# Optimization experiments

Hardware: AMD Instinct MI355X
Metric: run time of the kernel (lower is better)

Reference implementation:

```python
import jax, jax.numpy as jnp
import numpy as np

B, H, L = 8, 512, 8192


def setup_inputs() -> dict:
    key = jax.random.key(0)
    k1, k2, k3, k4 = jax.random.split(key, 4)
    u = jax.random.normal(k1, (B, H, L), dtype=jnp.float32)
    # SSM convolution kernel (decaying, as a Vandermonde 'Vr' kernel would be)
    decay = jnp.exp(-jnp.arange(L, dtype=jnp.float32) / 512.0)  # (L,)
    K = jax.random.normal(k2, (H, L), dtype=jnp.float32) * decay[None, :] / np.sqrt(L)
    D = jax.random.normal(k3, (H,), dtype=jnp.float32)
    W_mix = jax.random.normal(k4, (H, H), dtype=jnp.float32) / np.sqrt(H)
    return {"u": u, "K": K, "D": D, "W_mix": W_mix}


def reference(u, K, D, W_mix):
    # FFTConvReservoir: causal conv of u (B,H,L) with per-channel kernel K (H,L)
    n = 2 * L  # zero-pad to avoid circular wrap-around
    Uf = jnp.fft.rfft(u, n=n, axis=-1)            # (B,H,L+1) complex
    Kf = jnp.fft.rfft(K, n=n, axis=-1)            # (H,L+1) complex
    y = jnp.fft.irfft(Uf * Kf[None], n=n, axis=-1)[..., :L]
    y = y + D[None, :, None] * u                  # skip connection
    # LinearReservoir mix (frozen real matrix) applied pointwise over time
    y = jnp.einsum('ph,bhl->bpl', W_mix, y)
    # tanh nonlinearity
    y = jnp.tanh(y)
    return y
```

## Files before the change

### kernel.cpp

```cpp
#include <hip/hip_runtime.h>
#include <hip/hip_fp16.h>


#define FFT_N 8192
#define TAPS  4096
#define Bb 8
#define Hh 512
#define Ll 8192
#define NTHR 512

#define P(i) ((i) ^ (((i) >> 4) & 15))

__host__ __device__ constexpr int clog2(int x) { return x <= 1 ? 0 : 1 + clog2(x >> 1); }

typedef _Float16 half8 __attribute__((ext_vector_type(8)));
typedef _Float16 half2v __attribute__((ext_vector_type(2)));
typedef float f32x4 __attribute__((ext_vector_type(4)));

__device__ __forceinline__ float2 cmul(float2 a, float2 b) {
    return make_float2(a.x * b.x - a.y * b.y, a.x * b.y + a.y * b.x);
}
__device__ __forceinline__ float2 cmulc(float2 a, float2 b) {
    return make_float2(a.x * b.x + a.y * b.y, a.y * b.x - a.x * b.y);
}
__device__ __forceinline__ float2 cadd(float2 a, float2 b) { return make_float2(a.x + b.x, a.y + b.y); }
__device__ __forceinline__ float2 csub(float2 a, float2 b) { return make_float2(a.x - b.x, a.y - b.y); }

__device__ __forceinline__ float tanh_fast(float x) {
    float e = __expf(2.0f * x);
    return 1.0f - 2.0f / (e + 1.0f);
}

__device__ __forceinline__ void r4_fwd(float2& x0, float2& x1, float2& x2, float2& x3,
                                       float2 w1, float2 w2, float2 w3) {
    float2 t0 = cadd(x0, x2), t1 = csub(x0, x2), t2 = cadd(x1, x3), t3 = csub(x1, x3);
    x0 = cadd(t0, t2);
    x1 = cmul(make_float2(t1.x + t3.y, t1.y - t3.x), w1);
    x2 = cmul(csub(t0, t2), w2);
    x3 = cmul(make_float2(t1.x - t3.y, t1.y + t3.x), w3);
}
__device__ __forceinline__ void r4_fwd_nt(float2& x0, float2& x1, float2& x2, float2& x3) {
    float2 t0 = cadd(x0, x2), t1 = csub(x0, x2), t2 = cadd(x1, x3), t3 = csub(x1, x3);
    x0 = cadd(t0, t2);
    x1 = make_float2(t1.x + t3.y, t1.y - t3.x);
    x2 = csub(t0, t2);
    x3 = make_float2(t1.x - t3.y, t1.y + t3.x);
}
__device__ __forceinline__ void r4_inv(float2& x0, float2& x1, float2& x2, float2& x3,
                                       float2 w1, float2 w2, float2 w3) {
    float2 u1 = cmulc(x1, w1), u2 = cmulc(x2, w2), u3 = cmulc(x3, w3);
    float2 s0 = cadd(x0, u2), s2 = csub(x0, u2), s1 = cadd(u1, u3);
    float2 d = csub(u1, u3);
    float2 s3 = make_float2(-d.y, d.x);
    x0 = cadd(s0, s1); x1 = cadd(s2, s3); x2 = csub(s0, s1); x3 = csub(s2, s3);
}
__device__ __forceinline__ void r4_inv_nt(float2& x0, float2& x1, float2& x2, float2& x3) {
    float2 s0 = cadd(x0, x2), s2 = csub(x0, x2), s1 = cadd(x1, x3);
    float2 d = csub(x1, x3);
    float2 s3 = make_float2(-d.y, d.x);
    x0 = cadd(s0, s1); x1 = cadd(s2, s3); x2 = csub(s0, s1); x3 = csub(s2, s3);
}

template<int Q, int NT>
__device__ __forceinline__ void fwd_super(float2* buf, const float2* __restrict__ tw, int tid) {
    constexpr int q2 = Q / 4;
    constexpr int NB = 2048 / Q;
    constexpr int L2Q2 = clog2(q2);
    #pragma unroll 1
    for (int g = tid; g < 512; g += NT) {
        const int j = g & (q2 - 1);
        const int Bi = g >> L2Q2;
        const int base = Bi * 4 * Q + j;
        float2 x[4][4];
        #pragma unroll
        for (int a = 0; a < 4; ++a)
            #pragma unroll
            for (int b = 0; b < 4; ++b)
                x[a][b] = buf[P(base + a * Q + b * q2)];
        #pragma unroll
        for (int b = 0; b < 4; ++b) {
            float2 w1 = tw[(j + b * q2) * NB];
            float2 w2 = cmul(w1, w1), w3 = cmul(w2, w1);
            r4_fwd(x[0][b], x[1][b], x[2][b], x[3][b], w1, w2, w3);
        }
        {
            float2 v1 = tw[j * 4 * NB];
            float2 v2 = cmul(v1, v1), v3 = cmul(v2, v1);
            #pragma unroll
            for (int a = 0; a < 4; ++a)
                r4_fwd(x[a][0], x[a][1], x[a][2], x[a][3], v1, v2, v3);
        }
        #pragma unroll
        for (int a = 0; a < 4; ++a)
            #pragma unroll
            for (int b = 0; b < 4; ++b)
                buf[P(base + a * Q + b * q2)] = x[a][b];
    }
}

template<int Q, int NT>
__device__ __forceinline__ void inv_super(float2* buf, const float2* __restrict__ tw, int tid) {
    constexpr int q2 = Q / 4;
    constexpr int NB = 2048 / Q;
    constexpr int L2Q2 = clog2(q2);
    #pragma unroll 1
    for (int g = tid; g < 512; g += NT) {
        const int j = g & (q2 - 1);
        const int Bi = g >> L2Q2;
        const int base = Bi * 4 * Q + j;
        float2 x[4][4];
        #pragma unroll
        for (int a = 0; a < 4; ++a)
            #pragma unroll
            for (int b = 0; b < 4; ++b)
                x[a][b] = buf[P(base + a * Q + b * q2)];
        {
            float2 v1 = tw[j * 4 * NB];
            float2 v2 = cmul(v1, v1), v3 = cmul(v2, v1);
            #pragma unroll
            for (int a = 0; a < 4; ++a)
                r4_inv(x[a][0], x[a][1], x[a][2], x[a][3], v1, v2, v3);
        }
        #pragma unroll
        for (int b = 0; b < 4; ++b) {
            float2 w1 = tw[(j + b * q2) * NB];
            float2 w2 = cmul(w1, w1), w3 = cmul(w2, w1);
            r4_inv(x[0][b], x[1][b], x[2][b], x[3][b], w1, w2, w3);
        }
        #pragma unroll
        for (int a = 0; a < 4; ++a)
            #pragma unroll
            for (int b = 0; b < 4; ++b)
                buf[P(base + a * Q + b * q2)] = x[a][b];
    }
}

template<int NT>
__device__ __forceinline__ void mid_stage(float2* buf, const float2* __restrict__ kf, int tid) {
    const float2 W1[4] = {{1.f, 0.f}, {0.92387953f, -0.38268343f}, {0.70710678f, -0.70710678f}, {0.38268343f, -0.92387953f}};
    const float2 W2[4] = {{1.f, 0.f}, {0.70710678f, -0.70710678f}, {0.f, -1.f}, {-0.70710678f, -0.70710678f}};
    const float2 W3[4] = {{1.f, 0.f}, {0.38268343f, -0.92387953f}, {-0.70710678f, -0.70710678f}, {-0.92387953f, 0.38268343f}};
    #pragma unroll 1
    for (int g = tid; g < 512; g += NT) {
        const int base = 16 * g;
        float2 x[16];
        #pragma unroll
        for (int i = 0; i < 16; ++i) x[i] = buf[P(base + i)];
        #pragma unroll
        for (int b = 0; b < 4; ++b)
            r4_fwd(x[b], x[4 + b], x[8 + b], x[12 + b], W1[b], W2[b], W3[b]);
        #pragma unroll
        for (int a = 0; a < 4; ++a)
            r4_fwd_nt(x[4 * a], x[4 * a + 1], x[4 * a + 2], x[4 * a + 3]);
        const float4* kp = reinterpret_cast<const float4*>(kf + base);
        #pragma unroll
        for (int i = 0; i < 8; ++i) {
            float4 kv = kp[i];
            x[2 * i]     = cmul(x[2 * i],     make_float2(kv.x, kv.y));
            x[2 * i + 1] = cmul(x[2 * i + 1], make_float2(kv.z, kv.w));
        }
        #pragma unroll
        for (int a = 0; a < 4; ++a)
            r4_inv_nt(x[4 * a], x[4 * a + 1], x[4 * a + 2], x[4 * a + 3]);
        #pragma unroll
        for (int b = 0; b < 4; ++b)
            r4_inv(x[b], x[4 + b], x[8 + b], x[12 + b], W1[b], W2[b], W3[b]);
        #pragma unroll
        for (int i = 0; i < 16; ++i) buf[P(base + i)] = x[i];
    }
}

__global__ __launch_bounds__(256) void tw_init_kernel(float2* __restrict__ tw) {
    int k = blockIdx.x * 256 + threadIdx.x;
    if (k < FFT_N) {
        float s, c;
        sincospif(-(float)k / 4096.0f, &s, &c);
        tw[k] = make_float2(c, s);
    }
}

__global__ __launch_bounds__(256) void wh_kernel(const float* __restrict__ W, _Float16* __restrict__ Wh) {
    int i = blockIdx.x * 256 + threadIdx.x;
    Wh[i] = (_Float16)W[i];
}

__global__ __launch_bounds__(NTHR) void kf_kernel(const float* __restrict__ K,
                                                  const float* __restrict__ D,
                                                  const float2* __restrict__ tw,
                                                  float2* __restrict__ Kf) {
    __shared__ float2 buf[FFT_N];
    const int h = blockIdx.x;
    const int tid = threadIdx.x;
    for (int k = 0; k < 8; ++k) {
        int t = tid + k * NTHR;
        float va = (t < TAPS) ? K[(size_t)h * Ll + t] : 0.0f;
        if (t == 0) va += D[h];
        float2 a = make_float2(va, 0.0f);
        buf[P(t)] = a;
        buf[P(t + 4096)] = cmul(a, tw[t]);
    }
    __syncthreads();
    fwd_super<1024, NTHR>(buf, tw, tid);
    __syncthreads();
    fwd_super<64, NTHR>(buf, tw, tid);
    __syncthreads();
    fwd_super<4, NTHR>(buf, tw, tid);
    __syncthreads();
    for (int k = 0; k < 16; ++k) {
        int idx = tid + k * NTHR;
        Kf[(size_t)h * FFT_N + idx] = buf[P(idx)];
    }
}

__global__ __launch_bounds__(NTHR) void conv_kernel(const float* __restrict__ u,
                                                    const float2* __restrict__ Kf,
                                                    const float2* __restrict__ tw,
                                                    _Float16* __restrict__ yh) {
    __shared__ float2 buf[FFT_N];
    const int bid = blockIdx.x;
    const int h = bid & 511;
    const int pc = bid >> 9;
    const int c = pc & 1;
    const int bp = pc >> 1;
    const int b0 = bp * 2, b1 = b0 + 1;
    const int tid = threadIdx.x;
    const float* u0 = u + ((size_t)b0 * Hh + h) * Ll;
    const float* u1 = u + ((size_t)b1 * Hh + h) * Ll;
    const int t0 = c * 4096 - 4096;

    for (int k = 0; k < 8; ++k) {
        int t = tid + k * NTHR;
        int ta = t0 + t;
        float2 a = make_float2(0.f, 0.f);
        if (ta >= 0) a = make_float2(u0[ta], u1[ta]);
        int tb = ta + 4096;
        float2 bv = make_float2(u0[tb], u1[tb]);
        buf[P(t)] = cadd(a, bv);
        buf[P(t + 4096)] = cmul(csub(a, bv), tw[t]);
    }
    __syncthreads();
    fwd_super<1024, NTHR>(buf, tw, tid);
    __syncthreads();
    fwd_super<64, NTHR>(buf, tw, tid);
    __syncthreads();
    mid_stage<NTHR>(buf, Kf + (size_t)h * FFT_N, tid);
    __syncthreads();
    inv_super<64, NTHR>(buf, tw, tid);
    __syncthreads();
    inv_super<1024, NTHR>(buf, tw, tid);
    __syncthreads();

    const float scale = 1.0f / (float)FFT_N;
    _Float16* y0 = yh + ((size_t)b0 * Hh + h) * Ll;
    _Float16* y1 = yh + ((size_t)b1 * Hh + h) * Ll;
    for (int k = 0; k < 4; ++k) {
        int t = 2 * (tid + k * NTHR);
        float2 a0 = buf[P(t)],     c0 = buf[P(t + 4096)];
        float2 a1 = buf[P(t + 1)], c1 = buf[P(t + 4097)];
        float2 o0 = csub(a0, cmulc(c0, tw[t]));
        float2 o1 = csub(a1, cmulc(c1, tw[t + 1]));
        int l = c * 4096 + t;
        half2v h0, h1;
        h0.x = (_Float16)(o0.x * scale); h0.y = (_Float16)(o1.x * scale);
        h1.x = (_Float16)(o0.y * scale); h1.y = (_Float16)(o1.y * scale);
        *(half2v*)(y0 + l) = h0;
        *(half2v*)(y1 + l) = h1;
    }
}

__global__ __launch_bounds__(256) void transpose_kernel(const unsigned short* __restrict__ yh,
                                                        unsigned short* __restrict__ yt) {
    const int tid = threadIdx.x;
    const int b = blockIdx.z;
    const int h_base = blockIdx.y * 64 + (tid & 7) * 8;
    const int l_base = blockIdx.x * 256 + (tid >> 3) * 8;

    uint4 in[8];
    #pragma unroll
    for (int r = 0; r < 8; ++r)
        in[r] = *(const uint4*)(yh + (size_t)(b * Hh + h_base + r) * Ll + l_base);

    #pragma unroll
    for (int cp = 0; cp < 8; ++cp) {
        uint4 o;
        unsigned* ow = (unsigned*)&o;
        #pragma unroll
        for (int w = 0; w < 4; ++w) {
            unsigned lo = ((const unsigned*)&in[2 * w])[cp >> 1];
            unsigned hi = ((const unsigned*)&in[2 * w + 1])[cp >> 1];
            if (cp & 1) ow[w] = (lo >> 16) | (hi & 0xffff0000u);
            else        ow[w] = (lo & 0xffffu) | (hi << 16);
        }
        *(uint4*)(yt + ((size_t)b * Ll + l_base + cp) * Hh + h_base) = o;
    }
}

__global__ __launch_bounds__(256, 4) void mix_kernel(const _Float16* __restrict__ Wh,
                                                     const _Float16* __restrict__ yt,
                                                     float* __restrict__ out) {
    __shared__ _Float16 As[256 * 64];
    __shared__ _Float16 Bs[64 * 64];
    const int tid = threadIdx.x;
    const int lane = tid & 63;
    const int w = tid >> 6;
    const int m0 = blockIdx.y * 256;
    const int n0 = blockIdx.x * 64;
    const int b = blockIdx.z;
    const int wm = (w & 1) * 128;
    const int wn = (w >> 1) * 32;

    f32x4 acc[8][2];
    #pragma unroll
    for (int i = 0; i < 8; ++i)
        #pragma unroll
        for (int j = 0; j < 2; ++j)
            acc[i][j] = (f32x4){0.f, 0.f, 0.f, 0.f};

    const int lr = lane >> 3;
    const int cg = (lane & 7) ^ lr;
    const _Float16* gA0 = Wh + (size_t)(m0 + w * 64 + lr) * 512 + cg * 8;
    const _Float16* gB0 = yt + ((size_t)b * Ll + n0 + w * 16 + lr) * 512 + cg * 8;
    _Float16* lA0 = As + (w * 64) * 64;
    _Float16* lB0 = Bs + (w * 16) * 64;

    for (int k0 = 0; k0 < 512; k0 += 64) {
        __syncthreads();
        #pragma unroll
        for (int q = 0; q < 8; ++q)
            __builtin_amdgcn_global_load_lds(
                (const __attribute__((address_space(1))) void*)(gA0 + k0 + q * 8 * 512),
                (__attribute__((address_space(3))) void*)(lA0 + q * 8 * 64), 16, 0, 0);
        #pragma unroll
        for (int q = 0; q < 2; ++q)
            __builtin_amdgcn_global_load_lds(
                (const __attribute__((address_space(1))) void*)(gB0 + k0 + q * 8 * 512),
                (__attribute__((address_space(3))) void*)(lB0 + q * 8 * 64), 16, 0, 0);
        __syncthreads();
        #pragma unroll
        for (int kk = 0; kk < 2; ++kk) {
            const int cc = kk * 4 + (lane >> 4);
            half8 bf[2];
            #pragma unroll
            for (int j = 0; j < 2; ++j) {
                const int rowb = wn + j * 16 + (lane & 15);
                bf[j] = *(const half8*)(Bs + rowb * 64 + ((cc ^ (rowb & 7)) << 3));
            }
            #pragma unroll
            for (int i = 0; i < 8; ++i) {
                const int rowa = wm + i * 16 + (lane & 15);
                half8 af = *(const half8*)(As + rowa * 64 + ((cc ^ (rowa & 7)) << 3));
                #pragma unroll
                for (int j = 0; j < 2; ++j)
                    acc[i][j] = __builtin_amdgcn_mfma_f32_16x16x32_f16(af, bf[j], acc[i][j], 0, 0, 0);
            }
        }
    }

    const int pr = (lane >> 4) << 2;
    const int lc = lane & 15;
    for (int i = 0; i < 8; ++i) {
        for (int j = 0; j < 2; ++j) {
            int ll = n0 + wn + j * 16 + lc;
            float* op = out + ((size_t)b * Hh + (m0 + wm + i * 16 + pr)) * Ll + ll;
            for (int r = 0; r < 4; ++r)
                op[(size_t)r * Ll] = tanh_fast(acc[i][j][r]);
        }
    }
}

extern "C" void kernel_launch(void* const* d_in, const int* in_sizes, int n_in,
                              void* d_out, int out_size, void* d_ws, size_t ws_size,
                              hipStream_t stream) {
    const float* u = (const float*)d_in[0];
    const float* K = (const float*)d_in[1];
    const float* D = (const float*)d_in[2];
    const float* W = (const float*)d_in[3];

    char* ws = (char*)d_ws;
    float2*   Kf = (float2*)ws;
    float2*   tw = (float2*)(ws + (size_t)33554432);
    _Float16* Wh = (_Float16*)(ws + (size_t)33554432 + 65536);
    _Float16* yt = (_Float16*)(ws + (size_t)33554432 + 65536 + 524288);
    _Float16* yh = (_Float16*)d_out;
    float*   out = (float*)d_out;

    tw_init_kernel<<<32, 256, 0, stream>>>(tw);
    wh_kernel<<<1024, 256, 0, stream>>>(W, Wh);
    kf_kernel<<<512, NTHR, 0, stream>>>(K, D, tw, Kf);
    conv_kernel<<<4096, NTHR, 0, stream>>>(u, Kf, tw, yh);
    transpose_kernel<<<dim3(32, 8, 8), 256, 0, stream>>>((const unsigned short*)yh,
                                                         (unsigned short*)yt);
    mix_kernel<<<dim3(128, 2, 8), 256, 0, stream>>>(Wh, yt, out);
}
```

Baseline: 480.1 us.

## Fuse transpose into mix GEMM B-load, vectorize complex math, precompute twiddle powers

Removes the separate transpose kernel: the mix GEMM now reads the conv output in its (b,h,l) layout and transposes 4x4 fp16 tiles in registers while writing them to LDS, with an adjusted XOR swizzle. This cuts a full global round trip of the fp16 intermediate. The conv intermediate moves from the output buffer to workspace. Separately, complex arithmetic is rewritten on 2-wide float vectors, and twiddle powers w2 and w3 are loaded from the table rather than computed by multiplication. The grid-stride loops in the FFT stages are dropped on the assumption of exactly 512 threads. The cost is that the B tile is now loaded through registers instead of async global-to-LDS loads, with narrower 8-byte strided reads.

```diff
diff --git a/kernel.cpp b/kernel.cpp
--- a/kernel.cpp
+++ b/kernel.cpp
@@ -16,166 +16,159 @@
 typedef _Float16 half8 __attribute__((ext_vector_type(8)));
 typedef _Float16 half2v __attribute__((ext_vector_type(2)));
 typedef float f32x4 __attribute__((ext_vector_type(4)));
-
-__device__ __forceinline__ float2 cmul(float2 a, float2 b) {
-    return make_float2(a.x * b.x - a.y * b.y, a.x * b.y + a.y * b.x);
-}
-__device__ __forceinline__ float2 cmulc(float2 a, float2 b) {
-    return make_float2(a.x * b.x + a.y * b.y, a.y * b.x - a.x * b.y);
-}
-__device__ __forceinline__ float2 cadd(float2 a, float2 b) { return make_float2(a.x + b.x, a.y + b.y); }
-__device__ __forceinline__ float2 csub(float2 a, float2 b) { return make_float2(a.x - b.x, a.y - b.y); }
+typedef float cf2 __attribute__((ext_vector_type(2)));
+
+__device__ __forceinline__ cf2 cmul(cf2 a, cf2 b) {
+    cf2 br = {-b.y, b.x};
+    return b * a.x + br * a.y;
+}
+__device__ __forceinline__ cf2 cmulc(cf2 a, cf2 b) {
+    cf2 bc = {b.x, -b.y};
+    cf2 br = {b.y, b.x};
+    return bc * a.x + br * a.y;
+}
+__device__ __forceinline__ cf2 mul_negi(cf2 a) { return (cf2){a.y, -a.x}; }
+__device__ __forceinline__ cf2 mul_posi(cf2 a) { return (cf2){-a.y, a.x}; }
 
 __device__ __forceinline__ float tanh_fast(float x) {
     float e = __expf(2.0f * x);
     return 1.0f - 2.0f / (e + 1.0f);
 }
 
-__device__ __forceinline__ void r4_fwd(float2& x0, float2& x1, float2& x2, float2& x3,
-                                       float2 w1, float2 w2, float2 w3) {
-    float2 t0 = cadd(x0, x2), t1 = csub(x0, x2), t2 = cadd(x1, x3), t3 = csub(x1, x3);
-    x0 = cadd(t0, t2);
-    x1 = cmul(make_float2(t1.x + t3.y, t1.y - t3.x), w1);
-    x2 = cmul(csub(t0, t2), w2);
-    x3 = cmul(make_float2(t1.x - t3.y, t1.y + t3.x), w3);
-}
-__device__ __forceinline__ void r4_fwd_nt(float2& x0, float2& x1, float2& x2, float2& x3) {
-    float2 t0 = cadd(x0, x2), t1 = csub(x0, x2), t2 = cadd(x1, x3), t3 = csub(x1, x3);
-    x0 = cadd(t0, t2);
-    x1 = make_float2(t1.x + t3.y, t1.y - t3.x);
-    x2 = csub(t0, t2);
-    x3 = make_float2(t1.x - t3.y, t1.y + t3.x);
-}
-__device__ __forceinline__ void r4_inv(float2& x0, float2& x1, float2& x2, float2& x3,
-                                       float2 w1, float2 w2, float2 w3) {
-    float2 u1 = cmulc(x1, w1), u2 = cmulc(x2, w2), u3 = cmulc(x3, w3);
-    float2 s0 = cadd(x0, u2), s2 = csub(x0, u2), s1 = cadd(u1, u3);
-    float2 d = csub(u1, u3);
-    float2 s3 = make_float2(-d.y, d.x);
-    x0 = cadd(s0, s1); x1 = cadd(s2, s3); x2 = csub(s0, s1); x3 = csub(s2, s3);
-}
-__device__ __forceinline__ void r4_inv_nt(float2& x0, float2& x1, float2& x2, float2& x3) {
-    float2 s0 = cadd(x0, x2), s2 = csub(x0, x2), s1 = cadd(x1, x3);
-    float2 d = csub(x1, x3);
-    float2 s3 = make_float2(-d.y, d.x);
-    x0 = cadd(s0, s1); x1 = cadd(s2, s3); x2 = csub(s0, s1); x3 = csub(s2, s3);
-}
-
-template<int Q, int NT>
-__device__ __forceinline__ void fwd_super(float2* buf, const float2* __restrict__ tw, int tid) {
+__device__ __forceinline__ void r4_fwd(cf2& x0, cf2& x1, cf2& x2, cf2& x3,
+                                       cf2 w1, cf2 w2, cf2 w3) {
+    cf2 t0 = x0 + x2, t1 = x0 - x2, t2 = x1 + x3, t3 = x1 - x3;
+    x0 = t0 + t2;
+    x1 = cmul(t1 + mul_negi(t3), w1);
+    x2 = cmul(t0 - t2, w2);
+    x3 = cmul(t1 + mul_posi(t3), w3);
+}
+__device__ __forceinline__ void r4_fwd_nt(cf2& x0, cf2& x1, cf2& x2, cf2& x3) {
+    cf2 t0 = x0 + x2, t1 = x0 - x2, t2 = x1 + x3, t3 = x1 - x3;
+    x0 = t0 + t2;
+    x1 = t1 + mul_negi(t3);
+    x2 = t0 - t2;
+    x3 = t1 + mul_posi(t3);
+}
+__device__ __forceinline__ void r4_inv(cf2& x0, cf2& x1, cf2& x2, cf2& x3,
+                                       cf2 w1, cf2 w2, cf2 w3) {
+    cf2 u1 = cmulc(x1, w1), u2 = cmulc(x2, w2), u3 = cmulc(x3, w3);
+    cf2 s0 = x0 + u2, s2 = x0 - u2, s1 = u1 + u3;
+    cf2 s3 = mul_posi(u1 - u3);
+    x0 = s0 + s1; x1 = s2 + s3; x2 = s0 - s1; x3 = s2 - s3;
+}
+__device__ __forceinline__ void r4_inv_nt(cf2& x0, cf2& x1, cf2& x2, cf2& x3) {
+    cf2 s0 = x0 + x2, s2 = x0 - x2, s1 = x1 + x3;
+    cf2 s3 = mul_posi(x1 - x3);
+    x0 = s0 + s1; x1 = s2 + s3; x2 = s0 - s1; x3 = s2 - s3;
+}
+
+template<int Q>
+__device__ __forceinline__ void fwd_super(cf2* buf, const cf2* __restrict__ tw, int tid) {
     constexpr int q2 = Q / 4;
     constexpr int NB = 2048 / Q;
     constexpr int L2Q2 = clog2(q2);
-    #pragma unroll 1
-    for (int g = tid; g < 512; g += NT) {
-        const int j = g & (q2 - 1);
-        const int Bi = g >> L2Q2;
-        const int base = Bi * 4 * Q + j;
-        float2 x[4][4];
+    const int g = tid;
+    const int j = g & (q2 - 1);
+    const int Bi = g >> L2Q2;
+    const int base = Bi * 4 * Q + j;
+    cf2 x[4][4];
+    #pragma unroll
+    for (int a = 0; a < 4; ++a)
+        #pragma unroll
+        for (int b = 0; b < 4; ++b)
+            x[a][b] = buf[P(base + a * Q + b * q2)];
+    #pragma unroll
+    for (int b = 0; b < 4; ++b) {
+        const int m1 = (j + b * q2) * NB;
+        r4_fwd(x[0][b], x[1][b], x[2][b], x[3][b], tw[m1], tw[2 * m1], tw[3 * m1]);
+    }
+    {
+        const int mv = j * 4 * NB;
+        cf2 v1 = tw[mv], v2 = tw[2 * mv], v3 = tw[3 * mv];
         #pragma unroll
         for (int a = 0; a < 4; ++a)
-            #pragma unroll
-            for (int b = 0; b < 4; ++b)
-                x[a][b] = buf[P(base + a * Q + b * q2)];
-        #pragma unroll
-        for (int b = 0; b < 4; ++b) {
-            float2 w1 = tw[(j + b * q2) * NB];
-            float2 w2 = cmul(w1, w1), w3 = cmul(w2, w1);
-            r4_fwd(x[0][b], x[1][b], x[2][b], x[3][b], w1, w2, w3);
-        }
-        {
-            float2 v1 = tw[j * 4 * NB];
-            float2 v2 = cmul(v1, v1), v3 = cmul(v2, v1);
-            #pragma unroll
-            for (int a = 0; a < 4; ++a)
-                r4_fwd(x[a][0], x[a][1], x[a][2], x[a][3], v1, v2, v3);
-        }
-        #pragma unroll
-        for (int a = 0; a < 4; ++a)
-            #pragma unroll
-            for (int b = 0; b < 4; ++b)
-                buf[P(base + a * Q + b * q2)] = x[a][b];
-    }
-}
-
-template<int Q, int NT>
-__device__ __forceinline__ void inv_super(float2* buf, const float2* __restrict__ tw, int tid) {
+            r4_fwd(x[a][0], x[a][1], x[a][2], x[a][3], v1, v2, v3);
+    }
+    #pragma unroll
+    for (int a = 0; a < 4; ++a)
+        #pragma unroll
+        for (int b = 0; b < 4; ++b)
+            buf[P(base + a * Q + b * q2)] = x[a][b];
+}
+
+template<int Q>
+__device__ __forceinline__ void inv_super(cf2* buf, const cf2* __restrict__ tw, int tid) {
     constexpr int q2 = Q / 4;
     constexpr int NB = 2048 / Q;
     constexpr int L2Q2 = clog2(q2);
-    #pragma unroll 1
-    for (int g = tid; g < 512; g += NT) {
-        const int j = g & (q2 - 1);
-        const int Bi = g >> L2Q2;
-        const int base = Bi * 4 * Q + j;
-        float2 x[4][4];
+    const int g = tid;
+    const int j = g & (q2 - 1);
+    const int Bi = g >> L2Q2;
+    const int base = Bi * 4 * Q + j;
+    cf2 x[4][4];
+    #pragma unroll
+    for (int a = 0; a < 4; ++a)
+        #pragma unroll
+        for (int b = 0; b < 4; ++b)
+            x[a][b] = buf[P(base + a * Q + b * q2)];
+    {
+        const int mv = j * 4 * NB;
+        cf2 v1 = tw[mv], v2 = tw[2 * mv], v3 = tw[3 * mv];
         #pragma unroll
         for (int a = 0; a < 4; ++a)
-            #pragma unroll
-            for (int b = 0; b < 4; ++b)
-                x[a][b] = buf[P(base + a * Q + b * q2)];
-        {
-            float2 v1 = tw[j * 4 * NB];
-            float2 v2 = cmul(v1, v1), v3 = cmul(v2, v1);
-            #pragma unroll
-            for (int a = 0; a < 4; ++a)
-                r4_inv(x[a][0], x[a][1], x[a][2], x[a][3], v1, v2, v3);
-        }
-        #pragma unroll
-        for (int b = 0; b < 4; ++b) {
-            float2 w1 = tw[(j + b * q2) * NB];
-            float2 w2 = cmul(w1, w1), w3 = cmul(w2, w1);
-            r4_inv(x[0][b], x[1][b], x[2][b], x[3][b], w1, w2, w3);
-        }
-        #pragma unroll
-        for (int a = 0; a < 4; ++a)
-            #pragma unroll
-            for (int b = 0; b < 4; ++b)
-                buf[P(base + a * Q + b * q2)] = x[a][b];
-    }
-}
-
-template<int NT>
-__device__ __forceinline__ void mid_stage(float2* buf, const float2* __restrict__ kf, int tid) {
-    const float2 W1[4] = {{1.f, 0.f}, {0.92387953f, -0.38268343f}, {0.70710678f, -0.70710678f}, {0.38268343f, -0.92387953f}};
-    const float2 W2[4] = {{1.f, 0.f}, {0.70710678f, -0.70710678f}, {0.f, -1.f}, {-0.70710678f, -0.70710678f}};
-    const float2 W3[4] = {{1.f, 0.f}, {0.38268343f, -0.92387953f}, {-0.70710678f, -0.70710678f}, {-0.92387953f, 0.38268343f}};
-    #pragma unroll 1
-    for (int g = tid; g < 512; g += NT) {
-        const int base = 16 * g;
-        float2 x[16];
-        #pragma unroll
-        for (int i = 0; i < 16; ++i) x[i] = buf[P(base + i)];
+            r4_inv(x[a][0], x[a][1], x[a][2], x[a][3], v1, v2, v3);
+    }
+    #pragma unroll
+    for (int b = 0; b < 4; ++b) {
+        const int m1 = (j + b * q2) * NB;
+        r4_inv(x[0][b], x[1][b], x[2][b], x[3][b], tw[m1], tw[2 * m1], tw[3 * m1]);
+    }
+    #pragma unroll
+    for (int a = 0; a < 4; ++a)
         #pragma unroll
         for (int b = 0; b < 4; ++b)
-            r4_fwd(x[b], x[4 + b], x[8 + b], x[12 + b], W1[b], W2[b], W3[b]);
-        #pragma unroll
-        for (int a = 0; a < 4; ++a)
-            r4_fwd_nt(x[4 * a], x[4 * a + 1], x[4 * a + 2], x[4 * a + 3]);
-        const float4* kp = reinterpret_cast<const float4*>(kf + base);
-        #pragma unroll
-        for (int i = 0; i < 8; ++i) {
-            float4 kv = kp[i];
-            x[2 * i]     = cmul(x[2 * i],     make_float2(kv.x, kv.y));
-            x[2 * i + 1] = cmul(x[2 * i + 1], make_float2(kv.z, kv.w));
-        }
-        #pragma unroll
-        for (int a = 0; a < 4; ++a)
-            r4_inv_nt(x[4 * a], x[4 * a + 1], x[4 * a + 2], x[4 * a + 3]);
-        #pragma unroll
-        for (int b = 0; b < 4; ++b)
-            r4_inv(x[b], x[4 + b], x[8 + b], x[12 + b], W1[b], W2[b], W3[b]);
-        #pragma unroll
-        for (int i = 0; i < 16; ++i) buf[P(base + i)] = x[i];
-    }
-}
-
-__global__ __launch_bounds__(256) void tw_init_kernel(float2* __restrict__ tw) {
+            buf[P(base + a * Q + b * q2)] = x[a][b];
+}
+
+__device__ __forceinline__ void mid_stage(cf2* buf, const cf2* __restrict__ kf, int tid) {
+    const cf2 W1[4] = {{1.f, 0.f}, {0.92387953f, -0.38268343f}, {0.70710678f, -0.70710678f}, {0.38268343f, -0.92387953f}};
+    const cf2 W2[4] = {{1.f, 0.f}, {0.70710678f, -0.70710678f}, {0.f, -1.f}, {-0.70710678f, -0.70710678f}};
+    const cf2 W3[4] = {{1.f, 0.f}, {0.38268343f, -0.92387953f}, {-0.70710678f, -0.70710678f}, {-0.92387953f, 0.38268343f}};
+    const int g = tid;
+    const int base = 16 * g;
+    cf2 x[16];
+    #pragma unroll
+    for (int i = 0; i < 16; ++i) x[i] = buf[P(base + i)];
+    #pragma unroll
+    for (int b = 0; b < 4; ++b)
+        r4_fwd(x[b], x[4 + b], x[8 + b], x[12 + b], W1[b], W2[b], W3[b]);
+    #pragma unroll
+    for (int a = 0; a < 4; ++a)
+        r4_fwd_nt(x[4 * a], x[4 * a + 1], x[4 * a + 2], x[4 * a + 3]);
+    const float4* kp = reinterpret_cast<const float4*>(kf + base);
+    #pragma unroll
+    for (int i = 0; i < 8; ++i) {
+        float4 kv = kp[i];
+        x[2 * i]     = cmul(x[2 * i],     (cf2){kv.x, kv.y});
+        x[2 * i + 1] = cmul(x[2 * i + 1], (cf2){kv.z, kv.w});
+    }
+    #pragma unroll
+    for (int a = 0; a < 4; ++a)
+        r4_inv_nt(x[4 * a], x[4 * a + 1], x[4 * a + 2], x[4 * a + 3]);
+    #pragma unroll
+    for (int b = 0; b < 4; ++b)
+        r4_inv(x[b], x[4 + b], x[8 + b], x[12 + b], W1[b], W2[b], W3[b]);
+    #pragma unroll
+    for (int i = 0; i < 16; ++i) buf[P(base + i)] = x[i];
+}
+
+__global__ __launch_bounds__(256) void tw_init_kernel(cf2* __restrict__ tw) {
     int k = blockIdx.x * 256 + threadIdx.x;
     if (k < FFT_N) {
         float s, c;
         sincospif(-(float)k / 4096.0f, &s, &c);
-        tw[k] = make_float2(c, s);
+        tw[k] = (cf2){c, s};
     }
 }
 
@@ -186,25 +179,25 @@
 
 __global__ __launch_bounds__(NTHR) void kf_kernel(const float* __restrict__ K,
                                                   const float* __restrict__ D,
-                                                  const float2* __restrict__ tw,
-                                                  float2* __restrict__ Kf) {
-    __shared__ float2 buf[FFT_N];
+                                                  const cf2* __restrict__ tw,
+                                                  cf2* __restrict__ Kf) {
+    __shared__ cf2 buf[FFT_N];
     const int h = blockIdx.x;
     const int tid = threadIdx.x;
     for (int k = 0; k < 8; ++k) {
         int t = tid + k * NTHR;
         float va = (t < TAPS) ? K[(size_t)h * Ll + t] : 0.0f;
         if (t == 0) va += D[h];
-        float2 a = make_float2(va, 0.0f);
+        cf2 a = {va, 0.0f};
         buf[P(t)] = a;
         buf[P(t + 4096)] = cmul(a, tw[t]);
     }
     __syncthreads();
-    fwd_super<1024, NTHR>(buf, tw, tid);
-    __syncthreads();
-    fwd_super<64, NTHR>(buf, tw, tid);
-    __syncthreads();
-    fwd_super<4, NTHR>(buf, tw, tid);
+    fwd_super<1024>(buf, tw, tid);
+    __syncthreads();
+    fwd_super<64>(buf, tw, tid);
+    __syncthreads();
+    fwd_super<4>(buf, tw, tid);
     __syncthreads();
     for (int k = 0; k < 16; ++k) {
         int idx = tid + k * NTHR;
@@ -213,10 +206,10 @@
 }
 
 __global__ __launch_bounds__(NTHR) void conv_kernel(const float* __restrict__ u,
-                                                    const float2* __restrict__ Kf,
-                                                    const float2* __restrict__ tw,
+                                                    const cf2* __restrict__ Kf,
+                                                    const cf2* __restrict__ tw,
                                                     _Float16* __restrict__ yh) {
-    __shared__ float2 buf[FFT_N];
+    __shared__ cf2 buf[FFT_N];
     const int bid = blockIdx.x;
     const int h = bid & 511;
     const int pc = bid >> 9;
@@ -231,23 +224,23 @@
     for (int k = 0; k < 8; ++k) {
         int t = tid + k * NTHR;
         int ta = t0 + t;
-        float2 a = make_float2(0.f, 0.f);
-        if (ta >= 0) a = make_float2(u0[ta], u1[ta]);
+        cf2 a = {0.f, 0.f};
+        if (ta >= 0) a = (cf2){u0[ta], u1[ta]};
         int tb = ta + 4096;
-        float2 bv = make_float2(u0[tb], u1[tb]);
-        buf[P(t)] = cadd(a, bv);
-        buf[P(t + 4096)] = cmul(csub(a, bv), tw[t]);
-    }
-    __syncthreads();
-    fwd_super<1024, NTHR>(buf, tw, tid);
-    __syncthreads();
-    fwd_super<64, NTHR>(buf, tw, tid);
-    __syncthreads();
-    mid_stage<NTHR>(buf, Kf + (size_t)h * FFT_N, tid);
-    __syncthreads();
-    inv_super<64, NTHR>(buf, tw, tid);
-    __syncthreads();
-    inv_super<1024, NTHR>(buf, tw, tid);
+        cf2 bv = {u0[tb], u1[tb]};
+        buf[P(t)] = a + bv;
+        buf[P(t + 4096)] = cmul(a - bv, tw[t]);
+    }
+    __syncthreads();
+    fwd_super<1024>(buf, tw, tid);
+    __syncthreads();
+    fwd_super<64>(buf, tw, tid);
+    __syncthreads();
+    mid_stage(buf, Kf + (size_t)h * FFT_N, tid);
+    __syncthreads();
+    inv_super<64>(buf, tw, tid);
+    __syncthreads();
+    inv_super<1024>(buf, tw, tid);
     __syncthreads();
 
     const float scale = 1.0f / (float)FFT_N;
@@ -255,10 +248,10 @@
     _Float16* y1 = yh + ((size_t)b1 * Hh + h) * Ll;
     for (int k = 0; k < 4; ++k) {
         int t = 2 * (tid + k * NTHR);
-        float2 a0 = buf[P(t)],     c0 = buf[P(t + 4096)];
-        float2 a1 = buf[P(t + 1)], c1 = buf[P(t + 4097)];
-        float2 o0 = csub(a0, cmulc(c0, tw[t]));
-        float2 o1 = csub(a1, cmulc(c1, tw[t + 1]));
+        cf2 a0 = buf[P(t)],     c0 = buf[P(t + 4096)];
+        cf2 a1 = buf[P(t + 1)], c1 = buf[P(t + 4097)];
+        cf2 o0 = a0 - cmulc(c0, tw[t]);
+        cf2 o1 = a1 - cmulc(c1, tw[t + 1]);
         int l = c * 4096 + t;
         half2v h0, h1;
         h0.x = (_Float16)(o0.x * scale); h0.y = (_Float16)(o1.x * scale);
@@ -268,35 +261,8 @@
     }
 }
 
-__global__ __launch_bounds__(256) void transpose_kernel(const unsigned short* __restrict__ yh,
-                                                        unsigned short* __restrict__ yt) {
-    const int tid = threadIdx.x;
-    const int b = blockIdx.z;
-    const int h_base = blockIdx.y * 64 + (tid & 7) * 8;
-    const int l_base = blockIdx.x * 256 + (tid >> 3) * 8;
-
-    uint4 in[8];
-    #pragma unroll
-    for (int r = 0; r < 8; ++r)
-        in[r] = *(const uint4*)(yh + (size_t)(b * Hh + h_base + r) * Ll + l_base);
-
-    #pragma unroll
-    for (int cp = 0; cp < 8; ++cp) {
-        uint4 o;
-        unsigned* ow = (unsigned*)&o;
-        #pragma unroll
-        for (int w = 0; w < 4; ++w) {
-            unsigned lo = ((const unsigned*)&in[2 * w])[cp >> 1];
-            unsigned hi = ((const unsigned*)&in[2 * w + 1])[cp >> 1];
-            if (cp & 1) ow[w] = (lo >> 16) | (hi & 0xffff0000u);
-            else        ow[w] = (lo & 0xffffu) | (hi << 16);
-        }
-        *(uint4*)(yt + ((size_t)b * Ll + l_base + cp) * Hh + h_base) = o;
-    }
-}
-
 __global__ __launch_bounds__(256, 4) void mix_kernel(const _Float16* __restrict__ Wh,
-                                                     const _Float16* __restrict__ yt,
+                                                     const _Float16* __restrict__ yh,
                                                      float* __restrict__ out) {
     __shared__ _Float16 As[256 * 64];
     __shared__ _Float16 Bs[64 * 64];
@@ -317,11 +283,13 @@
             acc[i][j] = (f32x4){0.f, 0.f, 0.f, 0.f};
 
     const int lr = lane >> 3;
-    const int cg = (lane & 7) ^ lr;
-    const _Float16* gA0 = Wh + (size_t)(m0 + w * 64 + lr) * 512 + cg * 8;
-    const _Float16* gB0 = yt + ((size_t)b * Ll + n0 + w * 16 + lr) * 512 + cg * 8;
+    const int cgA = (lane & 7) ^ lr;
+    const _Float16* gA0 = Wh + (size_t)(m0 + w * 64 + lr) * 512 + cgA * 8;
     _Float16* lA0 = As + (w * 64) * 64;
-    _Float16* lB0 = Bs + (w * 16) * 64;
+
+    const int hq = tid >> 4;
+    const int lq = tid & 15;
+    const _Float16* gB0 = yh + ((size_t)b * Hh + hq * 4) * (size_t)Ll + n0 + lq * 4;
 
     for (int k0 = 0; k0 < 512; k0 += 64) {
         __syncthreads();
@@ -330,11 +298,21 @@
             __builtin_amdgcn_global_load_lds(
                 (const __attribute__((address_space(1))) void*)(gA0 + k0 + q * 8 * 512),
                 (__attribute__((address_space(3))) void*)(lA0 + q * 8 * 64), 16, 0, 0);
-        #pragma unroll
-        for (int q = 0; q < 2; ++q)
-            __builtin_amdgcn_global_load_lds(
-                (const __attribute__((address_space(1))) void*)(gB0 + k0 + q * 8 * 512),
-                (__attribute__((address_space(3))) void*)(lB0 + q * 8 * 64), 16, 0, 0);
+        uint2 in4[4];
+        #pragma unroll
+        for (int r = 0; r < 4; ++r)
+            in4[r] = *(const uint2*)(gB0 + (size_t)(k0 + r) * Ll);
+        const unsigned* iw = (const unsigned*)in4;
+        #pragma unroll
+        for (int cp = 0; cp < 4; ++cp) {
+            const int wsel = cp >> 1, sh = (cp & 1) * 16;
+            unsigned lo = ((iw[0 + wsel] >> sh) & 0xffffu) | (((iw[2 + wsel] >> sh) & 0xffffu) << 16);
+            unsigned hi = ((iw[4 + wsel] >> sh) & 0xffffu) | (((iw[6 + wsel] >> sh) & 0xffffu) << 16);
+            const int row = lq * 4 + cp;
+            const int f = (row ^ (row >> 3)) & 7;
+            const int ch = hq >> 1, sub = hq & 1;
+            *(uint2*)(Bs + row * 64 + ((ch ^ f) << 3) + sub * 4) = make_uint2(lo, hi);
+        }
         __syncthreads();
         #pragma unroll
         for (int kk = 0; kk < 2; ++kk) {
@@ -343,7 +321,8 @@
             #pragma unroll
             for (int j = 0; j < 2; ++j) {
                 const int rowb = wn + j * 16 + (lane & 15);
-                bf[j] = *(const half8*)(Bs + rowb * 64 + ((cc ^ (rowb & 7)) << 3));
+                const int fb = (rowb ^ (rowb >> 3)) & 7;
+                bf[j] = *(const half8*)(Bs + rowb * 64 + ((cc ^ fb) << 3));
             }
             #pragma unroll
             for (int i = 0; i < 8; ++i) {
@@ -377,18 +356,15 @@
     const float* W = (const float*)d_in[3];
 
     char* ws = (char*)d_ws;
-    float2*   Kf = (float2*)ws;
-    float2*   tw = (float2*)(ws + (size_t)33554432);
+    cf2*      Kf = (cf2*)ws;
+    cf2*      tw = (cf2*)(ws + (size_t)33554432);
     _Float16* Wh = (_Float16*)(ws + (size_t)33554432 + 65536);
-    _Float16* yt = (_Float16*)(ws + (size_t)33554432 + 65536 + 524288);
-    _Float16* yh = (_Float16*)d_out;
+    _Float16* yh = (_Float16*)(ws + (size_t)33554432 + 65536 + 524288);
     float*   out = (float*)d_out;
 
     tw_init_kernel<<<32, 256, 0, stream>>>(tw);
     wh_kernel<<<1024, 256, 0, stream>>>(W, Wh);
     kf_kernel<<<512, NTHR, 0, stream>>>(K, D, tw, Kf);
     conv_kernel<<<4096, NTHR, 0, stream>>>(u, Kf, tw, yh);
-    transpose_kernel<<<dim3(32, 8, 8), 256, 0, stream>>>((const unsigned short*)yh,
-                                                         (unsigned short*)yt);
-    mix_kernel<<<dim3(128, 2, 8), 256, 0, stream>>>(Wh, yt, out);
-}
+    mix_kernel<<<dim3(128, 2, 8), 256, 0, stream>>>(Wh, yh, out);
+}
```

After: 579.7 us. 1.21x slower.
